# Performance work log

Hardware: AMD Instinct MI355X
Metric: run time of the kernel (lower is better)

The kernel has to match this reference:

```python
import jax, jax.numpy as jnp
import numpy as np
import math

B, S, T = 32, 128, 64
FEAT = 16
H = 1024
V = 32000


def _gru_step(x, h, wih, whh, bih, bhh):
    # torch nn.GRU cell: gates ordered (r, z, n)
    gi = x @ wih.T + bih
    gh = h @ whh.T + bhh
    ir, iz, in_ = jnp.split(gi, 3, axis=-1)
    hr, hz, hn = jnp.split(gh, 3, axis=-1)
    r = jax.nn.sigmoid(ir + hr)
    z = jax.nn.sigmoid(iz + hz)
    n = jnp.tanh(in_ + r * hn)
    return (1.0 - z) * n + z * h


def _forward(features, target_tokens, temp_W, temp_b, hum_W, hum_b, cloud_W, cloud_b,
             time_W, time_b, other_W, other_b, fi_W, fi_b,
             enc_wih, enc_whh, enc_bih, enc_bhh, emb, attn_W, attn_b,
             dec_wih, dec_whh, dec_bih, dec_bhh, out_W, out_b):
    b = features.shape[0]
    # per-feature projections (dropout = identity in eval mode)
    temp = features[:, :, 0:1] @ temp_W.T + temp_b
    hum = features[:, :, 1:2] @ hum_W.T + hum_b
    cloud = features[:, :, 2:3] @ cloud_W.T + cloud_b
    time = features[:, :, -5:-3] @ time_W.T + time_b
    other_in = jnp.concatenate([features[:, :, 3:-5], features[:, :, -3:]], axis=2)
    other = other_in @ other_W.T + other_b
    concat = jnp.concatenate([temp, hum, cloud, time, other], axis=2)  # [B,S,2H]
    proj = jnp.tanh(concat @ fi_W.T + fi_b)  # [B,S,H]

    # encoder GRU over time
    def enc_step(h, x):
        h2 = _gru_step(x, h, enc_wih, enc_whh, enc_bih, enc_bhh)
        return h2, h2
    h0 = jnp.zeros((b, H), proj.dtype)
    h_last, enc_outs = jax.lax.scan(enc_step, h0, proj.transpose(1, 0, 2))
    enc_out = enc_outs.transpose(1, 0, 2)  # [B,S,H]

    # attention keys computed once (loop-invariant in the original)
    keys = enc_out @ attn_W.T + attn_b  # [B,S,H]
    scale = 1.0 / math.sqrt(H)

    # decoder: teacher_forcing_ratio = 1.0 -> input at step t is target_tokens[:, t-1]
    def dec_step(h, tok):
        e = emb[tok]  # [B,H]
        scores = jnp.einsum('bh,bsh->bs', h, keys) * scale
        w = jax.nn.softmax(scores, axis=-1)
        ctx = jnp.einsum('bs,bsh->bh', w, enc_out)
        x = jnp.concatenate([e, ctx], axis=-1)  # [B,2H]
        h2 = _gru_step(x, h, dec_wih, dec_whh, dec_bih, dec_bhh)
        pred = jnp.concatenate([h2, ctx], axis=-1) @ out_W.T + out_b  # [B,V]
        return h2, pred

    _, preds = jax.lax.scan(dec_step, h_last, target_tokens[:, :-1].T)  # [T-1,B,V]
    outputs = jnp.zeros((b, target_tokens.shape[1], V), preds.dtype)
    outputs = outputs.at[:, 0, target_tokens[0, 0]].set(1.0)
    outputs = outputs.at[:, 1:, :].set(preds.transpose(1, 0, 2))
    return outputs


def setup_inputs() -> dict:
    key = jax.random.key(0)
    ks = jax.random.split(key, 32)
    nrm = lambda k, sh: jax.random.normal(k, sh, jnp.float32) * 0.05
    Hq = H // 4
    d = {}
    d['features'] = jax.random.normal(ks[0], (B, S, FEAT), jnp.float32)
    d['target_tokens'] = jax.random.randint(ks[1], (B, T), 0, V, dtype=jnp.int32)
    d['temp_W'] = nrm(ks[2], (Hq, 1)); d['temp_b'] = nrm(ks[3], (Hq,))
    d['hum_W'] = nrm(ks[4], (Hq, 1)); d['hum_b'] = nrm(ks[5], (Hq,))
    d['cloud_W'] = nrm(ks[6], (Hq, 1)); d['cloud_b'] = nrm(ks[7], (Hq,))
    d['time_W'] = nrm(ks[8], (Hq, 2)); d['time_b'] = nrm(ks[9], (Hq,))
    d['other_W'] = nrm(ks[10], (H, FEAT - 5)); d['other_b'] = nrm(ks[11], (H,))
    d['fi_W'] = nrm(ks[12], (H, 2 * H)); d['fi_b'] = nrm(ks[13], (H,))
    d['enc_wih'] = nrm(ks[14], (3 * H, H)); d['enc_whh'] = nrm(ks[15], (3 * H, H))
    d['enc_bih'] = nrm(ks[16], (3 * H,)); d['enc_bhh'] = nrm(ks[17], (3 * H,))
    d['emb'] = nrm(ks[18], (V, H))
    d['attn_W'] = nrm(ks[19], (H, H)); d['attn_b'] = nrm(ks[20], (H,))
    d['dec_wih'] = nrm(ks[21], (3 * H, 2 * H)); d['dec_whh'] = nrm(ks[22], (3 * H, H))
    d['dec_bih'] = nrm(ks[23], (3 * H,)); d['dec_bhh'] = nrm(ks[24], (3 * H,))
    d['out_W'] = nrm(ks[25], (V, 2 * H)); d['out_b'] = nrm(ks[26], (V,))
    return d


def reference(features, target_tokens, temp_W, temp_b, hum_W, hum_b, cloud_W, cloud_b,
              time_W, time_b, other_W, other_b, fi_W, fi_b,
              enc_wih, enc_whh, enc_bih, enc_bhh, emb, attn_W, attn_b,
              dec_wih, dec_whh, dec_bih, dec_bhh, out_W, out_b):
    return _forward(features, target_tokens, temp_W, temp_b, hum_W, hum_b, cloud_W, cloud_b,
                    time_W, time_b, other_W, other_b, fi_W, fi_b,
                    enc_wih, enc_whh, enc_bih, enc_bhh, emb, attn_W, attn_b,
                    dec_wih, dec_whh, dec_bih, dec_bhh, out_W, out_b)
```

## Files before the change

### kernel.cpp

```cpp
#include <hip/hip_runtime.h>

typedef float f32x4 __attribute__((ext_vector_type(4)));
typedef __bf16 bf16x8 __attribute__((ext_vector_type(8)));

#define DI static __device__ __forceinline__

DI unsigned short f2bf(float f) {
  unsigned u = __float_as_uint(f);
  u = (u + 0x7fffu + ((u >> 16) & 1u)) >> 16;
  return (unsigned short)u;
}
DI unsigned pk2(float lo, float hi) {
  return (unsigned)f2bf(lo) | ((unsigned)f2bf(hi) << 16);
}
DI float bflo(unsigned u) { return __uint_as_float(u << 16); }
DI float bfhi(unsigned u) { return __uint_as_float(u & 0xffff0000u); }
DI float sigm(float x) { return 1.0f / (1.0f + expf(-x)); }

DI void gl_lds16(const unsigned short* g, unsigned short* l) {
  __builtin_amdgcn_global_load_lds(
      (const __attribute__((address_space(1))) unsigned int*)g,
      (__attribute__((address_space(3))) unsigned int*)l, 16, 0, 0);
}

DI void st32_sc1(unsigned* p, unsigned v) {
  __hip_atomic_store(p, v, __ATOMIC_RELAXED, __HIP_MEMORY_SCOPE_AGENT);
}
DI void st64_sc1(unsigned long long* p, unsigned long long v) {
  __hip_atomic_store(p, v, __ATOMIC_RELAXED, __HIP_MEMORY_SCOPE_AGENT);
}
DI int ldw(const int* p) {
  return __hip_atomic_load(p, __ATOMIC_RELAXED, __HIP_MEMORY_SCOPE_AGENT);
}
DI void stw(int* p, int v) {
  __hip_atomic_store(p, v, __ATOMIC_RELAXED, __HIP_MEMORY_SCOPE_AGENT);
}

DI void burn(int n) {
  float x = (float)(int)threadIdx.x;
#pragma unroll 1
  for (int i = 0; i < n; ++i) x = __builtin_fmaf(x, 1.0000001f, 1e-9f);
  asm volatile("" :: "v"(x));
}

DI void waitrel(const int* relbase, int repl, int target) {
  const int* w = relbase + repl * 32;
  for (;;) {
    int v = 0;
    if ((threadIdx.x & 63) == 0) v = ldw(w);
    v = __shfl(v, 0);
    if (v >= target) break;
    burn(60);
  }
  asm volatile("" ::: "memory");
}
DI void strel(int* relbase, int v) {
  int l = threadIdx.x & 63;
  if (l < 8) stw(relbase + l * 32, v);
}
DI void wait_arr32(const int* arr, int target) {
  const int l = (int)(threadIdx.x & 63);
  const int* p = arr + (l << 3);
  for (;;) {
    int v = (l < 32) ? ldw(p) : target;
    if (__all(v >= target)) break;
    burn(60);
  }
  asm volatile("" ::: "memory");
}

__global__ void k_fold(const float* __restrict__ tW, const float* __restrict__ tb,
                       const float* __restrict__ hW, const float* __restrict__ hb,
                       const float* __restrict__ cW, const float* __restrict__ cb,
                       const float* __restrict__ tiW, const float* __restrict__ tib,
                       const float* __restrict__ oW, const float* __restrict__ ob,
                       const float* __restrict__ fiW, const float* __restrict__ fib,
                       float* __restrict__ M, float* __restrict__ b0v)
{
  int g = blockIdx.x * 256 + threadIdx.x;
  if (g >= 1024 * 17) return;
  int h = g / 17, f = g - h * 17;
  const float* fw = fiW + (size_t)h * 2048;
  float s = 0.f;
  if (f == 16) {
    for (int k = 0; k < 256; ++k) s += fw[k] * tb[k];
    for (int k = 0; k < 256; ++k) s += fw[256 + k] * hb[k];
    for (int k = 0; k < 256; ++k) s += fw[512 + k] * cb[k];
    for (int k = 0; k < 256; ++k) s += fw[768 + k] * tib[k];
    for (int r = 0; r < 1024; ++r) s += fw[1024 + r] * ob[r];
    b0v[h] = s + fib[h];
  } else if (f == 0) {
    for (int k = 0; k < 256; ++k) s += fw[k] * tW[k];
    M[h * 16 + 0] = s;
  } else if (f == 1) {
    for (int k = 0; k < 256; ++k) s += fw[256 + k] * hW[k];
    M[h * 16 + 1] = s;
  } else if (f == 2) {
    for (int k = 0; k < 256; ++k) s += fw[512 + k] * cW[k];
    M[h * 16 + 2] = s;
  } else if (f == 11) {
    for (int k = 0; k < 256; ++k) s += fw[768 + k] * tiW[2 * k];
    M[h * 16 + 11] = s;
  } else if (f == 12) {
    for (int k = 0; k < 256; ++k) s += fw[768 + k] * tiW[2 * k + 1];
    M[h * 16 + 12] = s;
  } else {
    int col = (f <= 10) ? (f - 3) : (f - 5);
    for (int r = 0; r < 1024; ++r) s += fw[1024 + r] * oW[r * 11 + col];
    M[h * 16 + f] = s;
  }
}

__global__ __launch_bounds__(256)
void k_proj(const float* __restrict__ feat, const float* __restrict__ M,
            const float* __restrict__ b0v, unsigned short* __restrict__ proj)
{
  __shared__ float ft[16];
  int bs = blockIdx.x;
  int h = blockIdx.y * 256 + threadIdx.x;
  if (threadIdx.x < 16) ft[threadIdx.x] = feat[bs * 16 + threadIdx.x];
  __syncthreads();
  float sum = b0v[h];
  const float* mr = M + h * 16;
#pragma unroll
  for (int f = 0; f < 16; ++f) sum += mr[f] * ft[f];
  proj[(size_t)bs * 1024 + h] = f2bf(tanhf(sum));
}

__global__ void k_conv(const float* __restrict__ s, unsigned short* __restrict__ d, int n8)
{
  for (long i = (long)blockIdx.x * 256 + threadIdx.x; i < n8; i += (long)gridDim.x * 256) {
    const float* p = s + i * 8;
    f32x4 a = *(const f32x4*)p, b = *(const f32x4*)(p + 4);
    uint4 o;
    o.x = pk2(a[0], a[1]); o.y = pk2(a[2], a[3]);
    o.z = pk2(b[0], b[1]); o.w = pk2(b[2], b[3]);
    *(uint4*)(d + i * 8) = o;
  }
}

__global__ void k_conv_str(const float* __restrict__ s, unsigned short* __restrict__ d, int coff)
{
  int r = blockIdx.x;
  int c = threadIdx.x * 4;
  f32x4 a = *(const f32x4*)(s + (size_t)r * 2048 + coff + c);
  uint2 o; o.x = pk2(a[0], a[1]); o.y = pk2(a[2], a[3]);
  *(uint2*)(d + (size_t)r * 1024 + c) = o;
}

__global__ void k_gather_e(const int* __restrict__ toks, const float* __restrict__ emb,
                           unsigned short* __restrict__ e_bf)
{
  int row = blockIdx.x;
  int t = row >> 5, b = row & 31;
  unsigned short* dst = e_bf + (size_t)row * 1024 + threadIdx.x * 4;
  if (t < 63) {
    int tok = toks[b * 64 + t];
    f32x4 a = *(const f32x4*)(emb + (size_t)tok * 1024 + threadIdx.x * 4);
    uint2 o; o.x = pk2(a[0], a[1]); o.y = pk2(a[2], a[3]);
    *(uint2*)dst = o;
  } else {
    uint2 o; o.x = 0u; o.y = 0u;
    *(uint2*)dst = o;
  }
}

__global__ void k_onehot(const int* __restrict__ toks, float* __restrict__ out)
{
  int i = blockIdx.x * 256 + threadIdx.x;
  if (i >= 32 * 32000) return;
  int b = i / 32000, v = i - b * 32000;
  out[(size_t)b * 64 * 32000 + v] = (v == toks[0]) ? 1.0f : 0.0f;
}

template<int MODE>
__global__ __launch_bounds__(256)
void gemm_bf(const unsigned short* __restrict__ A, const unsigned short* __restrict__ B,
             const float* __restrict__ bias, float* __restrict__ Cf,
             unsigned short* __restrict__ Cb,
             int tiles_m, int K, int lda, int ldb, int ldc, int coloff)
{
  __shared__ unsigned short As[4096];
  __shared__ unsigned short Bs[4096];
  const int nblk = gridDim.x;
  const int cpx = nblk >> 3;
  const int bid = blockIdx.x;
  const int id = (bid & 7) * cpx + (bid >> 3);
  const int tm = id % tiles_m, tn = id / tiles_m;
  const int tid = threadIdx.x;
  const int lane = tid & 63, wave = tid >> 6;
  const int wm = (wave & 1) << 6, wn = (wave >> 1) << 6;
  const int r0 = tid >> 2, kc0 = (tid & 3) << 3;
  const unsigned short* ga0 = A + (size_t)(tm * 128 + r0) * lda + kc0;
  const unsigned short* ga1 = A + (size_t)(tm * 128 + 64 + r0) * lda + kc0;
  const unsigned short* gb0 = B + (size_t)(tn * 128 + r0) * ldb + kc0;
  const unsigned short* gb1 = B + (size_t)(tn * 128 + 64 + r0) * ldb + kc0;
  const int lr = lane & 15, lkb = (lane >> 4) << 3;

  f32x4 acc[4][4];
#pragma unroll
  for (int m = 0; m < 4; ++m)
#pragma unroll
    for (int n = 0; n < 4; ++n) { acc[m][n][0]=0.f; acc[m][n][1]=0.f; acc[m][n][2]=0.f; acc[m][n][3]=0.f; }

  for (int kt = 0; kt < K; kt += 32) {
    __syncthreads();
    gl_lds16(ga0 + kt, &As[tid * 8]);
    gl_lds16(ga1 + kt, &As[(tid + 256) * 8]);
    gl_lds16(gb0 + kt, &Bs[tid * 8]);
    gl_lds16(gb1 + kt, &Bs[(tid + 256) * 8]);
    __syncthreads();
    bf16x8 af[4], bfv[4];
#pragma unroll
    for (int m = 0; m < 4; ++m) af[m] = *(const bf16x8*)&As[(wm + m * 16 + lr) * 32 + lkb];
#pragma unroll
    for (int n = 0; n < 4; ++n) bfv[n] = *(const bf16x8*)&Bs[(wn + n * 16 + lr) * 32 + lkb];
#pragma unroll
    for (int m = 0; m < 4; ++m)
#pragma unroll
      for (int n = 0; n < 4; ++n)
        acc[m][n] = __builtin_amdgcn_mfma_f32_16x16x32_bf16(af[m], bfv[n], acc[m][n], 0, 0, 0);
  }

#pragma unroll
  for (int m = 0; m < 4; ++m) {
    int rb = tm * 128 + wm + m * 16 + ((lane >> 4) << 2);
#pragma unroll
    for (int n = 0; n < 4; ++n) {
      int c = tn * 128 + wn + n * 16 + lr;
      float bb = bias[c];
#pragma unroll
      for (int i = 0; i < 4; ++i) {
        float v = acc[m][n][i] + bb;
        int r = rb + i;
        if (MODE == 0) {
          Cf[(size_t)r * ldc + c] = v;
        } else if (MODE == 1) {
          Cb[(size_t)r * ldc + c] = f2bf(v);
        } else if (MODE == 3) {
          Cb[(size_t)c * 4096 + r] = f2bf(v);
        } else {
          if (r < 2016) {
            int t = r >> 5, b2 = r & 31;
            Cf[((size_t)b2 * 64 + t + 1) * 32000 + coloff + c] = v;
          }
        }
      }
    }
  }
}

__global__ __launch_bounds__(256, 1)
void k_enc_scan(const float* __restrict__ gi_all, const float* __restrict__ whh,
                const float* __restrict__ bhh, float* __restrict__ hfp,
                unsigned short* __restrict__ enc_bf,
                int* __restrict__ arrE, int* __restrict__ relE)
{
  const int tid = threadIdx.x;
  const int blk = blockIdx.x;
  if (blk == 64) {
    if (tid < 64) {
      for (int g = 1; g <= 127; ++g) {
        for (;;) {
          int v = ldw(&arrE[tid << 3]);
          if (__all(v >= g)) break;
          burn(60);
        }
        asm volatile("" ::: "memory");
        strel(relE, g);
      }
    }
    return;
  }

  __shared__ unsigned short W[48 * 1024];
  __shared__ float Cred[4 * 2 * 3 * 64 * 4];
  const int lane = tid & 63, wave = tid >> 6;
  const int j0 = blk * 16;
  const int repl = blk & 7;

  for (int i = tid; i < 48 * 128; i += 256) {
    int r = i >> 7, c = i & 127;
    int gr = ((r >> 4) << 10) + j0 + (r & 15);
    const float* src = whh + ((size_t)gr << 10) + (c << 3);
    f32x4 a = *(const f32x4*)src, b = *(const f32x4*)(src + 4);
    uint4 o;
    o.x = pk2(a[0], a[1]); o.y = pk2(a[2], a[3]);
    o.z = pk2(b[0], b[1]); o.w = pk2(b[2], b[3]);
    *(uint4*)&W[(r << 10) + ((c ^ (r & 7)) << 3)] = o;
  }
  __syncthreads();

  int cb[2], cj[2], clb[2], creg[2], cm[2];
  float bh0[2], bh1[2], bh2[2];
  float hp[2] = {0.f, 0.f};
#pragma unroll
  for (int cc = 0; cc < 2; ++cc) {
    int cell = tid + (cc << 8);
    cb[cc] = cell >> 4; cj[cc] = cell & 15;
    clb[cc] = ((cb[cc] & 15) >> 2) * 16;
    creg[cc] = cb[cc] & 3; cm[cc] = cb[cc] >> 4;
    bh0[cc] = bhh[j0 + cj[cc]];
    bh1[cc] = bhh[1024 + j0 + cj[cc]];
    bh2[cc] = bhh[2048 + j0 + cj[cc]];
  }

#pragma unroll 1
  for (int s = 0; s < 128; ++s) {
    float gp[2][3];
#pragma unroll
    for (int cc = 0; cc < 2; ++cc) {
      const float* gi = gi_all + ((size_t)cb[cc] * 128 + s) * 3072 + j0 + cj[cc];
      gp[cc][0] = gi[0]; gp[cc][1] = gi[1024]; gp[cc][2] = gi[2048];
    }

    f32x4 acc[2][3];
#pragma unroll
    for (int m = 0; m < 2; ++m)
#pragma unroll
      for (int n = 0; n < 3; ++n) { acc[m][n][0]=0.f; acc[m][n][1]=0.f; acc[m][n][2]=0.f; acc[m][n][3]=0.f; }

    if (s > 0) {
      waitrel(relE, repl, s);
      const unsigned short* hr = enc_bf + (size_t)(s - 1) * 1024;
      const int k0 = wave << 8;
      bf16x8 af[2][8];
#pragma unroll
      for (int kk = 0; kk < 8; ++kk) {
        int k = k0 + kk * 32 + ((lane >> 4) << 3);
        af[0][kk] = *(const bf16x8*)(hr + (size_t)(lane & 15) * 131072 + k);
        af[1][kk] = *(const bf16x8*)(hr + (size_t)(16 + (lane & 15)) * 131072 + k);
      }
#pragma unroll
      for (int kk = 0; kk < 8; ++kk) {
        int c = ((k0 + kk * 32) >> 3) + (lane >> 4);
#pragma unroll
        for (int n = 0; n < 3; ++n) {
          int wr = n * 16 + (lane & 15);
          bf16x8 bfr = *(const bf16x8*)&W[(wr << 10) + ((c ^ (wr & 7)) << 3)];
          acc[0][n] = __builtin_amdgcn_mfma_f32_16x16x32_bf16(af[0][kk], bfr, acc[0][n], 0, 0, 0);
          acc[1][n] = __builtin_amdgcn_mfma_f32_16x16x32_bf16(af[1][kk], bfr, acc[1][n], 0, 0, 0);
        }
      }
    }
#pragma unroll
    for (int m = 0; m < 2; ++m)
#pragma unroll
      for (int n = 0; n < 3; ++n)
        *(f32x4*)&Cred[((((wave * 2 + m) * 3 + n) * 64) + lane) << 2] = acc[m][n];
    __syncthreads();

    float h2v[2];
#pragma unroll
    for (int cc = 0; cc < 2; ++cc) {
      int lj = clb[cc] + cj[cc], reg = creg[cc], m = cm[cc];
      float Cr = 0.f, Cz = 0.f, Cn = 0.f;
#pragma unroll
      for (int w = 0; w < 4; ++w) {
        Cr += Cred[((((w * 2 + m) * 3 + 0) * 64 + lj) << 2) + reg];
        Cz += Cred[((((w * 2 + m) * 3 + 1) * 64 + lj) << 2) + reg];
        Cn += Cred[((((w * 2 + m) * 3 + 2) * 64 + lj) << 2) + reg];
      }
      float r = sigm(gp[cc][0] + Cr + bh0[cc]);
      float z = sigm(gp[cc][1] + Cz + bh1[cc]);
      float n = tanhf(gp[cc][2] + r * (Cn + bh2[cc]));
      float h2 = (1.f - z) * n + z * hp[cc];
      h2v[cc] = h2; hp[cc] = h2;
    }
    if (s == 127) {
      hfp[cb[0] * 1024 + j0 + cj[0]] = h2v[0];
      hfp[cb[1] * 1024 + j0 + cj[1]] = h2v[1];
    }
#pragma unroll
    for (int cc = 0; cc < 2; ++cc) {
      unsigned short sv = f2bf(h2v[cc]);
      unsigned p = (unsigned)sv | (((unsigned)__shfl_xor((int)(unsigned)sv, 1)) << 16);
      unsigned q = (unsigned)__shfl_xor((int)p, 2);
      if ((tid & 3) == 0) {
        unsigned long long dv = (unsigned long long)p | ((unsigned long long)q << 32);
        st64_sc1((unsigned long long*)&enc_bf[((size_t)cb[cc] * 128 + s) * 1024 + j0 + cj[cc]], dv);
      }
    }
    __syncthreads();
    if (tid == 0) stw(&arrE[blk << 3], s + 1);
  }
}

__global__ __launch_bounds__(256, 1)
void k_dec_scan(const float* __restrict__ gi_e, const float* __restrict__ whh,
                const float* __restrict__ bhh,
                const unsigned short* __restrict__ keys,
                const unsigned short* __restrict__ enc_bf,
                unsigned short* __restrict__ hcat, const float* __restrict__ hfp0,
                const unsigned short* __restrict__ xeT, float* __restrict__ w_all,
                int* __restrict__ arrW, int* __restrict__ arrH,
                int* __restrict__ relH)
{
  const int tid = threadIdx.x;
  const int blk = blockIdx.x;
  const int repl = blk & 7;

  if (blk == 160) {
    if (tid < 64) {
      for (int g = 1; g <= 62; ++g) {
        for (;;) {
          int v0 = ldw(&arrH[(tid * 2) << 4]);
          int v1 = ldw(&arrH[(tid * 2 + 1) << 4]);
          if (__all(v0 >= g && v1 >= g)) break;
          burn(60);
        }
        asm volatile("" ::: "memory");
        strel(relH, g);
      }
    }
    return;
  }

  if (blk < 32) {
    __shared__ unsigned short hsh[1024];
    __shared__ float sarr[128];
    __shared__ float earr[128];
    const int b = blk;
#pragma unroll 1
    for (int t = 0; t < 63; ++t) {
      if (t) waitrel(relH, repl, t);
      const unsigned short* hsrc = (t == 0)
          ? (enc_bf + (size_t)b * 131072 + (size_t)127 * 1024)
          : (hcat + ((size_t)(t - 1) * 32 + b) * 2048);
      *(uint2*)&hsh[tid * 4] = *(const uint2*)(hsrc + tid * 4);
      __syncthreads();
      {
        int sp = tid >> 1, kh = (tid & 1) << 9;
        const unsigned short* kr = keys + ((size_t)b * 128 + sp) * 1024 + kh;
        float a0 = 0.f, a1 = 0.f, a2 = 0.f, a3 = 0.f;
#pragma unroll 8
        for (int c = 0; c < 512; c += 8) {
          uint4 kv = *(const uint4*)(kr + c);
          uint4 hv = *(const uint4*)&hsh[kh + c];
          a0 += bflo(kv.x) * bflo(hv.x) + bfhi(kv.x) * bfhi(hv.x);
          a1 += bflo(kv.y) * bflo(hv.y) + bfhi(kv.y) * bfhi(hv.y);
          a2 += bflo(kv.z) * bflo(hv.z) + bfhi(kv.z) * bfhi(hv.z);
          a3 += bflo(kv.w) * bflo(hv.w) + bfhi(kv.w) * bfhi(hv.w);
        }
        float a = (a0 + a1) + (a2 + a3);
        a += __shfl_xor(a, 1);
        if ((tid & 1) == 0) sarr[sp] = a * 0.03125f;
      }
      __syncthreads();
      float m0 = -1e30f, m1 = -1e30f, m2 = -1e30f, m3 = -1e30f;
#pragma unroll 8
      for (int i2 = 0; i2 < 128; i2 += 4) {
        m0 = fmaxf(m0, sarr[i2]); m1 = fmaxf(m1, sarr[i2 + 1]);
        m2 = fmaxf(m2, sarr[i2 + 2]); m3 = fmaxf(m3, sarr[i2 + 3]);
      }
      float mx = fmaxf(fmaxf(m0, m1), fmaxf(m2, m3));
      if (tid < 128) earr[tid] = expf(sarr[tid] - mx);
      __syncthreads();
      float s0 = 0.f, s1 = 0.f, s2 = 0.f, s3 = 0.f;
#pragma unroll 8
      for (int i2 = 0; i2 < 128; i2 += 4) {
        s0 += earr[i2]; s1 += earr[i2 + 1]; s2 += earr[i2 + 2]; s3 += earr[i2 + 3];
      }
      float winv = 1.f / ((s0 + s1) + (s2 + s3));
      if (tid < 64) {
        unsigned lo = __float_as_uint(earr[tid * 2] * winv);
        unsigned hi = __float_as_uint(earr[tid * 2 + 1] * winv);
        st64_sc1((unsigned long long*)(w_all + ((size_t)t * 32 + b) * 128 + tid * 2),
                 (unsigned long long)lo | ((unsigned long long)hi << 32));
      }
      __syncthreads();
      if (tid == 0) stw(&arrW[b << 3], t + 1);
      f32x4 cacc; cacc[0]=0.f; cacc[1]=0.f; cacc[2]=0.f; cacc[3]=0.f;
      const unsigned short* eb = enc_bf + ((size_t)b << 17) + tid * 4;
#pragma unroll 4
      for (int s2i = 0; s2i < 128; ++s2i) {
        float w = earr[s2i] * winv;
        uint2 ev = *(const uint2*)(eb + ((size_t)s2i << 10));
        cacc[0] += w * bflo(ev.x); cacc[1] += w * bfhi(ev.x);
        cacc[2] += w * bflo(ev.y); cacc[3] += w * bfhi(ev.y);
      }
      uint2 co; co.x = pk2(cacc[0], cacc[1]); co.y = pk2(cacc[2], cacc[3]);
      *(uint2*)(hcat + ((size_t)t * 32 + b) * 2048 + 1024 + tid * 4) = co;
    }
    return;
  }

  __shared__ unsigned short Wh[32 * 1024];
  __shared__ float Cred[4 * 2 * 2 * 64 * 4];
  const int lane = tid & 63, wave = tid >> 6;
  const int gblk = blk - 32;
  const int j0 = gblk * 8;

  for (int i = tid; i < 32 * 128; i += 256) {
    int r = i >> 7, c = i & 127;
    int off = (r << 10) + ((c ^ (r & 7)) << 3);
    uint4 oh;
    oh.x = oh.y = oh.z = oh.w = 0u;
    if (r < 24) {
      int gr = ((r >> 3) << 10) + j0 + (r & 7);
      const float* sh = whh + ((size_t)gr << 10) + (c << 3);
      f32x4 a = *(const f32x4*)sh, b = *(const f32x4*)(sh + 4);
      oh.x = pk2(a[0], a[1]); oh.y = pk2(a[2], a[3]);
      oh.z = pk2(b[0], b[1]); oh.w = pk2(b[2], b[3]);
    }
    *(uint4*)&Wh[off] = oh;
  }
  __syncthreads();

  const int gb = tid >> 3, gj = tid & 7;
  const int glb = ((gb & 15) >> 2) * 16;
  const int greg = gb & 3, gm = gb >> 4;
  const float bh0 = bhh[j0 + gj];
  const float bh1 = bhh[1024 + j0 + gj];
  const float bh2 = bhh[2048 + j0 + gj];
  float hpv = hfp0[gb * 1024 + j0 + gj];
  const unsigned short* x0 = xeT + ((size_t)(j0 + gj) << 12) + gb * 128;
  const unsigned short* x1 = xeT + ((size_t)(1024 + j0 + gj) << 12) + gb * 128;
  const unsigned short* x2 = xeT + ((size_t)(2048 + j0 + gj) << 12) + gb * 128;

#pragma unroll 1
  for (int t = 0; t < 63; ++t) {
    const float* gie = gi_e + ((size_t)t * 32 + gb) * 3072 + j0 + gj;
    float g0 = gie[0], g1 = gie[1024], g2 = gie[2048];

    if (t) waitrel(relH, repl, t);
    const unsigned short* abase;
    size_t astr;
    if (t == 0) { abase = enc_bf + (size_t)127 * 1024; astr = 131072; }
    else { abase = hcat + (size_t)(t - 1) * 32 * 2048; astr = 2048; }
    const int k0 = wave << 8;
    f32x4 acc[2][2];
#pragma unroll
    for (int m = 0; m < 2; ++m)
#pragma unroll
      for (int n = 0; n < 2; ++n) { acc[m][n][0]=0.f; acc[m][n][1]=0.f; acc[m][n][2]=0.f; acc[m][n][3]=0.f; }
    {
      bf16x8 af[2][8];
#pragma unroll
      for (int kk = 0; kk < 8; ++kk) {
        int k = k0 + kk * 32 + ((lane >> 4) << 3);
        af[0][kk] = *(const bf16x8*)(abase + (size_t)(lane & 15) * astr + k);
        af[1][kk] = *(const bf16x8*)(abase + (size_t)(16 + (lane & 15)) * astr + k);
      }
#pragma unroll
      for (int kk = 0; kk < 8; ++kk) {
        int c = ((k0 + kk * 32) >> 3) + (lane >> 4);
#pragma unroll
        for (int n = 0; n < 2; ++n) {
          int wr = n * 16 + (lane & 15);
          bf16x8 bfr = *(const bf16x8*)&Wh[(wr << 10) + ((c ^ (wr & 7)) << 3)];
          acc[0][n] = __builtin_amdgcn_mfma_f32_16x16x32_bf16(af[0][kk], bfr, acc[0][n], 0, 0, 0);
          acc[1][n] = __builtin_amdgcn_mfma_f32_16x16x32_bf16(af[1][kk], bfr, acc[1][n], 0, 0, 0);
        }
      }
    }
#pragma unroll
    for (int m = 0; m < 2; ++m)
#pragma unroll
      for (int n = 0; n < 2; ++n)
        *(f32x4*)&Cred[((((wave * 2 + m) * 2 + n) * 64) + lane) << 2] = acc[m][n];
    __syncthreads();

    wait_arr32(arrW, t + 1);
    float cx0 = 0.f, cx1 = 0.f, cx2 = 0.f;
    const float* wrow = w_all + ((size_t)t * 32 + gb) * 128;
#pragma unroll 4
    for (int s = 0; s < 128; s += 8) {
      f32x4 wa = *(const f32x4*)(wrow + s);
      f32x4 wb2 = *(const f32x4*)(wrow + s + 4);
      uint4 a0 = *(const uint4*)(x0 + s);
      uint4 a1 = *(const uint4*)(x1 + s);
      uint4 a2 = *(const uint4*)(x2 + s);
      cx0 += wa[0]*bflo(a0.x) + wa[1]*bfhi(a0.x) + wa[2]*bflo(a0.y) + wa[3]*bfhi(a0.y)
           + wb2[0]*bflo(a0.z) + wb2[1]*bfhi(a0.z) + wb2[2]*bflo(a0.w) + wb2[3]*bfhi(a0.w);
      cx1 += wa[0]*bflo(a1.x) + wa[1]*bfhi(a1.x) + wa[2]*bflo(a1.y) + wa[3]*bfhi(a1.y)
           + wb2[0]*bflo(a1.z) + wb2[1]*bfhi(a1.z) + wb2[2]*bflo(a1.w) + wb2[3]*bfhi(a1.w);
      cx2 += wa[0]*bflo(a2.x) + wa[1]*bfhi(a2.x) + wa[2]*bflo(a2.y) + wa[3]*bfhi(a2.y)
           + wb2[0]*bflo(a2.z) + wb2[1]*bfhi(a2.z) + wb2[2]*bflo(a2.w) + wb2[3]*bfhi(a2.w);
    }

    {
      float Chr = 0.f, Chz = 0.f, Chn = 0.f;
#pragma unroll
      for (int w = 0; w < 4; ++w) {
        Chr += Cred[((((w * 2 + gm) * 2 + 0) * 64 + glb + gj) << 2) + greg];
        Chz += Cred[((((w * 2 + gm) * 2 + 0) * 64 + glb + gj + 8) << 2) + greg];
        Chn += Cred[((((w * 2 + gm) * 2 + 1) * 64 + glb + gj) << 2) + greg];
      }
      float r = sigm(g0 + cx0 + Chr + bh0);
      float z = sigm(g1 + cx1 + Chz + bh1);
      float n2 = tanhf(g2 + cx2 + r * (Chn + bh2));
      float h2 = (1.f - z) * n2 + z * hpv;
      hpv = h2;
      unsigned short sv = f2bf(h2);
      unsigned p = (unsigned)sv | (((unsigned)__shfl_xor((int)(unsigned)sv, 1)) << 16);
      unsigned q = (unsigned)__shfl_xor((int)p, 2);
      if ((tid & 3) == 0) {
        unsigned long long dv = (unsigned long long)p | ((unsigned long long)q << 32);
        st64_sc1((unsigned long long*)&hcat[((size_t)t * 32 + gb) * 2048 + j0 + gj], dv);
      }
    }
    __syncthreads();
    if (tid == 0) stw(&arrH[gblk << 4], t + 1);
  }
}

extern "C" void kernel_launch(void* const* d_in, const int* in_sizes, int n_in,
                              void* d_out, int out_size, void* d_ws, size_t ws_size,
                              hipStream_t stream)
{
  const float* features = (const float*)d_in[0];
  const int*   toks     = (const int*)d_in[1];
  const float* temp_W = (const float*)d_in[2];  const float* temp_b = (const float*)d_in[3];
  const float* hum_W  = (const float*)d_in[4];  const float* hum_b  = (const float*)d_in[5];
  const float* cloud_W= (const float*)d_in[6];  const float* cloud_b= (const float*)d_in[7];
  const float* time_W = (const float*)d_in[8];  const float* time_b = (const float*)d_in[9];
  const float* other_W= (const float*)d_in[10]; const float* other_b= (const float*)d_in[11];
  const float* fi_W   = (const float*)d_in[12]; const float* fi_b   = (const float*)d_in[13];
  const float* enc_wih= (const float*)d_in[14]; const float* enc_whh= (const float*)d_in[15];
  const float* enc_bih= (const float*)d_in[16]; const float* enc_bhh= (const float*)d_in[17];
  const float* emb    = (const float*)d_in[18];
  const float* attn_W = (const float*)d_in[19]; const float* attn_b = (const float*)d_in[20];
  const float* dec_wih= (const float*)d_in[21]; const float* dec_whh= (const float*)d_in[22];
  const float* dec_bih= (const float*)d_in[23]; const float* dec_bhh= (const float*)d_in[24];
  const float* out_W  = (const float*)d_in[25]; const float* out_b  = (const float*)d_in[26];
  float* out = (float*)d_out;
  char* ws = (char*)d_ws;

  int*            arrE    = (int*)(ws + 0);
  int*            arrH    = (int*)(ws + 4096);
  int*            arrW    = (int*)(ws + 12288);
  int*            relE    = (int*)(ws + 14336);
  int*            relH    = (int*)(ws + 15360);
  float*          zbias   = (float*)(ws + 16384);
  float*          Mf      = (float*)(ws + 32768);
  float*          b0v     = (float*)(ws + 98304);
  float*          hfp     = (float*)(ws + 102400);
  unsigned short* hcat    = (unsigned short*)(ws + 233472);
  unsigned short* keys_bf = (unsigned short*)(ws + 8622080);
  unsigned short* enc_bf  = (unsigned short*)(ws + 17010688);
  float*          w_all   = (float*)(ws + 25399296);
  float*          gi_e    = (float*)(ws + 26447872);
  unsigned short* xeT     = (unsigned short*)(ws + 51613696);
  float*          gi_all  = (float*)(ws + 76779520);
  unsigned short* proj_bf = (unsigned short*)(ws + 127111168);
  unsigned short* e_bf    = (unsigned short*)(ws + 135499776);
  unsigned short* wihE_bf = (unsigned short*)(ws + 139694080);
  unsigned short* attnW_bf= (unsigned short*)(ws + 145985536);
  unsigned short* wihD_bf = (unsigned short*)(ws + 148082688);
  unsigned short* wihDc_bf= (unsigned short*)(ws + 154374144);
  unsigned short* outW_bf = (unsigned short*)(ws + 26447872);

  hipMemsetAsync(ws, 0, 32768, stream);
  hipMemsetAsync(ws + 233472 + (size_t)2016 * 2048 * 2, 0, 32 * 2048 * 2, stream);

  k_conv<<<1536, 256, 0, stream>>>(enc_wih, wihE_bf, 393216);
  k_conv<<<512, 256, 0, stream>>>(attn_W, attnW_bf, 131072);
  k_conv_str<<<3072, 256, 0, stream>>>(dec_wih, wihD_bf, 0);
  k_conv_str<<<3072, 256, 0, stream>>>(dec_wih, wihDc_bf, 1024);

  k_fold<<<68, 256, 0, stream>>>(temp_W, temp_b, hum_W, hum_b, cloud_W, cloud_b,
                                 time_W, time_b, other_W, other_b, fi_W, fi_b, Mf, b0v);
  k_proj<<<dim3(4096, 4), 256, 0, stream>>>(features, Mf, b0v, proj_bf);

  gemm_bf<0><<<768, 256, 0, stream>>>(proj_bf, wihE_bf, enc_bih, gi_all, nullptr,
                                      32, 1024, 1024, 1024, 3072, 0);
  k_enc_scan<<<65, 256, 0, stream>>>(gi_all, enc_whh, enc_bhh, hfp, enc_bf, arrE, relE);

  gemm_bf<1><<<256, 256, 0, stream>>>(enc_bf, attnW_bf, attn_b, nullptr, keys_bf,
                                      32, 1024, 1024, 1024, 1024, 0);
  k_gather_e<<<2048, 256, 0, stream>>>(toks, emb, e_bf);
  gemm_bf<0><<<384, 256, 0, stream>>>(e_bf, wihD_bf, dec_bih, gi_e, nullptr,
                                      16, 1024, 1024, 1024, 3072, 0);
  gemm_bf<3><<<768, 256, 0, stream>>>(enc_bf, wihDc_bf, zbias, nullptr, xeT,
                                      32, 1024, 1024, 1024, 0, 0);
  k_dec_scan<<<161, 256, 0, stream>>>(gi_e, dec_whh, dec_bhh, keys_bf, enc_bf,
                                      hcat, hfp, xeT, w_all, arrW, arrH, relH);

  k_conv<<<2048, 256, 0, stream>>>(out_W, outW_bf, 4096000);
  gemm_bf<2><<<2000, 256, 0, stream>>>(hcat, outW_bf, out_b, out, nullptr,
                                       16, 2048, 2048, 2048, 0, 0);
  k_conv<<<2048, 256, 0, stream>>>(out_W + (size_t)16000 * 2048, outW_bf, 4096000);
  gemm_bf<2><<<2000, 256, 0, stream>>>(hcat, outW_bf, out_b + 16000, out, nullptr,
                                       16, 2048, 2048, 2048, 0, 16000);
  k_onehot<<<4000, 256, 0, stream>>>(toks, out);
}
```

Baseline: 2.910 ms.

## Split attention across blocks, cache keys in LDS, defer context to separate kernel

The decoder scan now uses two attention blocks per batch row, each holding 64 key rows in swizzled LDS, and writes unnormalized exp scores without a max subtraction. The per-step context computation over enc_out is moved out of the serial loop into a new batched k_ctx kernel. The GRU blocks keep xeT rows in registers and normalize by the score sum themselves. A relay block now publishes two-phase release counters for the attention and hidden-state stages. The aim is to shorten the serial critical path per step, at the cost of softmax overflow risk without the max subtraction and higher register pressure.

```diff
diff --git a/kernel.cpp b/kernel.cpp
--- a/kernel.cpp
+++ b/kernel.cpp
@@ -57,16 +57,6 @@
 DI void strel(int* relbase, int v) {
   int l = threadIdx.x & 63;
   if (l < 8) stw(relbase + l * 32, v);
-}
-DI void wait_arr32(const int* arr, int target) {
-  const int l = (int)(threadIdx.x & 63);
-  const int* p = arr + (l << 3);
-  for (;;) {
-    int v = (l < 32) ? ldw(p) : target;
-    if (__all(v >= target)) break;
-    burn(60);
-  }
-  asm volatile("" ::: "memory");
 }
 
 __global__ void k_fold(const float* __restrict__ tW, const float* __restrict__ tb,
@@ -394,101 +384,97 @@
                 unsigned short* __restrict__ hcat, const float* __restrict__ hfp0,
                 const unsigned short* __restrict__ xeT, float* __restrict__ w_all,
                 int* __restrict__ arrW, int* __restrict__ arrH,
-                int* __restrict__ relH)
-{
+                int* __restrict__ relD)
+{
+  static __shared__ __attribute__((aligned(16))) char smem[135168];
   const int tid = threadIdx.x;
   const int blk = blockIdx.x;
   const int repl = blk & 7;
 
-  if (blk == 160) {
+  if (blk == 192) {
     if (tid < 64) {
-      for (int g = 1; g <= 62; ++g) {
+      for (int t = 0; t < 63; ++t) {
+        for (;;) {
+          int v = ldw(&arrW[tid << 3]);
+          if (__all(v >= t + 1)) break;
+          burn(60);
+        }
+        asm volatile("" ::: "memory");
+        strel(relD, 2 * t + 1);
         for (;;) {
           int v0 = ldw(&arrH[(tid * 2) << 4]);
           int v1 = ldw(&arrH[(tid * 2 + 1) << 4]);
-          if (__all(v0 >= g && v1 >= g)) break;
+          if (__all(v0 >= t + 1 && v1 >= t + 1)) break;
           burn(60);
         }
         asm volatile("" ::: "memory");
-        strel(relH, g);
+        strel(relD, 2 * t + 2);
       }
     }
     return;
   }
 
-  if (blk < 32) {
-    __shared__ unsigned short hsh[1024];
-    __shared__ float sarr[128];
-    __shared__ float earr[128];
-    const int b = blk;
+  if (blk < 64) {
+    unsigned short* Ks = (unsigned short*)smem;
+    unsigned short* hsh = (unsigned short*)(smem + 131072);
+    float* parr = (float*)(smem + 133120);
+    const int b = blk >> 1, half = blk & 1;
+    const int lane = tid & 63, wave = tid >> 6;
+
+    for (int i = tid; i < 64 * 128; i += 256) {
+      int s = i >> 7, c = i & 127;
+      uint4 kv = *(const uint4*)(keys + ((size_t)(b * 128 + half * 64 + s) << 10) + (c << 3));
+      *(uint4*)&Ks[(s << 10) + ((c ^ (s & 7)) << 3)] = kv;
+    }
+    __syncthreads();
+
 #pragma unroll 1
     for (int t = 0; t < 63; ++t) {
-      if (t) waitrel(relH, repl, t);
+      if (t) waitrel(relD, repl, 2 * t);
       const unsigned short* hsrc = (t == 0)
           ? (enc_bf + (size_t)b * 131072 + (size_t)127 * 1024)
           : (hcat + ((size_t)(t - 1) * 32 + b) * 2048);
       *(uint2*)&hsh[tid * 4] = *(const uint2*)(hsrc + tid * 4);
       __syncthreads();
-      {
-        int sp = tid >> 1, kh = (tid & 1) << 9;
-        const unsigned short* kr = keys + ((size_t)b * 128 + sp) * 1024 + kh;
-        float a0 = 0.f, a1 = 0.f, a2 = 0.f, a3 = 0.f;
+      float a0 = 0.f, a1 = 0.f;
 #pragma unroll 8
-        for (int c = 0; c < 512; c += 8) {
-          uint4 kv = *(const uint4*)(kr + c);
-          uint4 hv = *(const uint4*)&hsh[kh + c];
-          a0 += bflo(kv.x) * bflo(hv.x) + bfhi(kv.x) * bfhi(hv.x);
-          a1 += bflo(kv.y) * bflo(hv.y) + bfhi(kv.y) * bfhi(hv.y);
-          a2 += bflo(kv.z) * bflo(hv.z) + bfhi(kv.z) * bfhi(hv.z);
-          a3 += bflo(kv.w) * bflo(hv.w) + bfhi(kv.w) * bfhi(hv.w);
+      for (int i = 0; i < 32; i += 2) {
+        int c0 = wave * 32 + i, c1 = c0 + 1;
+        uint4 kv0 = *(const uint4*)&Ks[(lane << 10) + ((c0 ^ (lane & 7)) << 3)];
+        uint4 kv1 = *(const uint4*)&Ks[(lane << 10) + ((c1 ^ (lane & 7)) << 3)];
+        uint4 hv0 = *(const uint4*)&hsh[c0 << 3];
+        uint4 hv1 = *(const uint4*)&hsh[c1 << 3];
+        a0 += bflo(kv0.x) * bflo(hv0.x) + bfhi(kv0.x) * bfhi(hv0.x)
+            + bflo(kv0.y) * bflo(hv0.y) + bfhi(kv0.y) * bfhi(hv0.y)
+            + bflo(kv0.z) * bflo(hv0.z) + bfhi(kv0.z) * bfhi(hv0.z)
+            + bflo(kv0.w) * bflo(hv0.w) + bfhi(kv0.w) * bfhi(hv0.w);
+        a1 += bflo(kv1.x) * bflo(hv1.x) + bfhi(kv1.x) * bfhi(hv1.x)
+            + bflo(kv1.y) * bflo(hv1.y) + bfhi(kv1.y) * bfhi(hv1.y)
+            + bflo(kv1.z) * bflo(hv1.z) + bfhi(kv1.z) * bfhi(hv1.z)
+            + bflo(kv1.w) * bflo(hv1.w) + bfhi(kv1.w) * bfhi(hv1.w);
+      }
+      parr[wave * 64 + lane] = a0 + a1;
+      __syncthreads();
+      if (tid < 64) {
+        float sc = (parr[tid] + parr[64 + tid] + parr[128 + tid] + parr[192 + tid]) * 0.03125f;
+        float e = expf(sc);
+        float eo = __shfl_xor(e, 1);
+        if ((tid & 1) == 0) {
+          unsigned long long dv = (unsigned long long)__float_as_uint(e)
+                                | ((unsigned long long)__float_as_uint(eo) << 32);
+          st64_sc1((unsigned long long*)(w_all + ((size_t)t * 32 + b) * 128 + half * 64 + tid), dv);
         }
-        float a = (a0 + a1) + (a2 + a3);
-        a += __shfl_xor(a, 1);
-        if ((tid & 1) == 0) sarr[sp] = a * 0.03125f;
       }
       __syncthreads();
-      float m0 = -1e30f, m1 = -1e30f, m2 = -1e30f, m3 = -1e30f;
-#pragma unroll 8
-      for (int i2 = 0; i2 < 128; i2 += 4) {
-        m0 = fmaxf(m0, sarr[i2]); m1 = fmaxf(m1, sarr[i2 + 1]);
-        m2 = fmaxf(m2, sarr[i2 + 2]); m3 = fmaxf(m3, sarr[i2 + 3]);
-      }
-      float mx = fmaxf(fmaxf(m0, m1), fmaxf(m2, m3));
-      if (tid < 128) earr[tid] = expf(sarr[tid] - mx);
-      __syncthreads();
-      float s0 = 0.f, s1 = 0.f, s2 = 0.f, s3 = 0.f;
-#pragma unroll 8
-      for (int i2 = 0; i2 < 128; i2 += 4) {
-        s0 += earr[i2]; s1 += earr[i2 + 1]; s2 += earr[i2 + 2]; s3 += earr[i2 + 3];
-      }
-      float winv = 1.f / ((s0 + s1) + (s2 + s3));
-      if (tid < 64) {
-        unsigned lo = __float_as_uint(earr[tid * 2] * winv);
-        unsigned hi = __float_as_uint(earr[tid * 2 + 1] * winv);
-        st64_sc1((unsigned long long*)(w_all + ((size_t)t * 32 + b) * 128 + tid * 2),
-                 (unsigned long long)lo | ((unsigned long long)hi << 32));
-      }
-      __syncthreads();
-      if (tid == 0) stw(&arrW[b << 3], t + 1);
-      f32x4 cacc; cacc[0]=0.f; cacc[1]=0.f; cacc[2]=0.f; cacc[3]=0.f;
-      const unsigned short* eb = enc_bf + ((size_t)b << 17) + tid * 4;
-#pragma unroll 4
-      for (int s2i = 0; s2i < 128; ++s2i) {
-        float w = earr[s2i] * winv;
-        uint2 ev = *(const uint2*)(eb + ((size_t)s2i << 10));
-        cacc[0] += w * bflo(ev.x); cacc[1] += w * bfhi(ev.x);
-        cacc[2] += w * bflo(ev.y); cacc[3] += w * bfhi(ev.y);
-      }
-      uint2 co; co.x = pk2(cacc[0], cacc[1]); co.y = pk2(cacc[2], cacc[3]);
-      *(uint2*)(hcat + ((size_t)t * 32 + b) * 2048 + 1024 + tid * 4) = co;
+      if (tid == 0) stw(&arrW[blk << 3], t + 1);
     }
     return;
   }
 
-  __shared__ unsigned short Wh[32 * 1024];
-  __shared__ float Cred[4 * 2 * 2 * 64 * 4];
+  unsigned short* Wh = (unsigned short*)smem;
+  float* Cred = (float*)(smem + 65536);
   const int lane = tid & 63, wave = tid >> 6;
-  const int gblk = blk - 32;
+  const int gblk = blk - 64;
   const int j0 = gblk * 8;
 
   for (int i = tid; i < 32 * 128; i += 256) {
@@ -514,16 +500,26 @@
   const float bh1 = bhh[1024 + j0 + gj];
   const float bh2 = bhh[2048 + j0 + gj];
   float hpv = hfp0[gb * 1024 + j0 + gj];
-  const unsigned short* x0 = xeT + ((size_t)(j0 + gj) << 12) + gb * 128;
-  const unsigned short* x1 = xeT + ((size_t)(1024 + j0 + gj) << 12) + gb * 128;
-  const unsigned short* x2 = xeT + ((size_t)(2048 + j0 + gj) << 12) + gb * 128;
+
+  uint4 x0v[16], x1v[16], x2v[16];
+  {
+    const unsigned short* x0 = xeT + ((size_t)(j0 + gj) << 12) + gb * 128;
+    const unsigned short* x1 = xeT + ((size_t)(1024 + j0 + gj) << 12) + gb * 128;
+    const unsigned short* x2 = xeT + ((size_t)(2048 + j0 + gj) << 12) + gb * 128;
+#pragma unroll
+    for (int i = 0; i < 16; ++i) {
+      x0v[i] = *(const uint4*)(x0 + i * 8);
+      x1v[i] = *(const uint4*)(x1 + i * 8);
+      x2v[i] = *(const uint4*)(x2 + i * 8);
+    }
+  }
 
 #pragma unroll 1
   for (int t = 0; t < 63; ++t) {
     const float* gie = gi_e + ((size_t)t * 32 + gb) * 3072 + j0 + gj;
     float g0 = gie[0], g1 = gie[1024], g2 = gie[2048];
 
-    if (t) waitrel(relH, repl, t);
+    if (t) waitrel(relD, repl, 2 * t);
     const unsigned short* abase;
     size_t astr;
     if (t == 0) { abase = enc_bf + (size_t)127 * 1024; astr = 131072; }
@@ -561,16 +557,15 @@
         *(f32x4*)&Cred[((((wave * 2 + m) * 2 + n) * 64) + lane) << 2] = acc[m][n];
     __syncthreads();
 
-    wait_arr32(arrW, t + 1);
-    float cx0 = 0.f, cx1 = 0.f, cx2 = 0.f;
+    waitrel(relD, repl, 2 * t + 1);
     const float* wrow = w_all + ((size_t)t * 32 + gb) * 128;
-#pragma unroll 4
-    for (int s = 0; s < 128; s += 8) {
-      f32x4 wa = *(const f32x4*)(wrow + s);
-      f32x4 wb2 = *(const f32x4*)(wrow + s + 4);
-      uint4 a0 = *(const uint4*)(x0 + s);
-      uint4 a1 = *(const uint4*)(x1 + s);
-      uint4 a2 = *(const uint4*)(x2 + s);
+    float se = 0.f, cx0 = 0.f, cx1 = 0.f, cx2 = 0.f;
+#pragma unroll
+    for (int i = 0; i < 16; ++i) {
+      f32x4 wa = *(const f32x4*)(wrow + i * 8);
+      f32x4 wb2 = *(const f32x4*)(wrow + i * 8 + 4);
+      se += (wa[0] + wa[1]) + (wa[2] + wa[3]) + (wb2[0] + wb2[1]) + (wb2[2] + wb2[3]);
+      uint4 a0 = x0v[i], a1 = x1v[i], a2 = x2v[i];
       cx0 += wa[0]*bflo(a0.x) + wa[1]*bfhi(a0.x) + wa[2]*bflo(a0.y) + wa[3]*bfhi(a0.y)
            + wb2[0]*bflo(a0.z) + wb2[1]*bfhi(a0.z) + wb2[2]*bflo(a0.w) + wb2[3]*bfhi(a0.w);
       cx1 += wa[0]*bflo(a1.x) + wa[1]*bfhi(a1.x) + wa[2]*bflo(a1.y) + wa[3]*bfhi(a1.y)
@@ -578,6 +573,8 @@
       cx2 += wa[0]*bflo(a2.x) + wa[1]*bfhi(a2.x) + wa[2]*bflo(a2.y) + wa[3]*bfhi(a2.y)
            + wb2[0]*bflo(a2.z) + wb2[1]*bfhi(a2.z) + wb2[2]*bflo(a2.w) + wb2[3]*bfhi(a2.w);
     }
+    float inv = 1.f / se;
+    cx0 *= inv; cx1 *= inv; cx2 *= inv;
 
     {
       float Chr = 0.f, Chz = 0.f, Chn = 0.f;
@@ -602,6 +599,54 @@
     }
     __syncthreads();
     if (tid == 0) stw(&arrH[gblk << 4], t + 1);
+  }
+}
+
+__global__ __launch_bounds__(256)
+void k_ctx(const float* __restrict__ w_all, const unsigned short* __restrict__ enc_bf,
+           unsigned short* __restrict__ hcat)
+{
+  __shared__ float wsh[8][128];
+  __shared__ float inv[8];
+  const int b = blockIdx.x, tg = blockIdx.y;
+  const int t0 = tg * 8;
+  const int nt = (t0 + 8 <= 63) ? 8 : (63 - t0);
+  const int tid = threadIdx.x;
+  for (int idx = tid; idx < 8 * 128; idx += 256) {
+    int tt = idx >> 7, s = idx & 127;
+    wsh[tt][s] = (tt < nt) ? w_all[((size_t)(t0 + tt) * 32 + b) * 128 + s] : 0.f;
+  }
+  __syncthreads();
+  if (tid < 8) {
+    float s = 0.f;
+    for (int i = 0; i < 128; ++i) s += wsh[tid][i];
+    inv[tid] = (tid < nt) ? 1.f / s : 0.f;
+  }
+  __syncthreads();
+  const int j0 = tid * 4;
+  f32x4 cacc[8];
+#pragma unroll
+  for (int tt = 0; tt < 8; ++tt) { cacc[tt][0]=0.f; cacc[tt][1]=0.f; cacc[tt][2]=0.f; cacc[tt][3]=0.f; }
+  const unsigned short* eb = enc_bf + ((size_t)b << 17) + j0;
+  for (int s = 0; s < 128; ++s) {
+    uint2 ev = *(const uint2*)(eb + ((size_t)s << 10));
+    float v0 = bflo(ev.x), v1 = bfhi(ev.x), v2 = bflo(ev.y), v3 = bfhi(ev.y);
+#pragma unroll
+    for (int tt = 0; tt < 8; ++tt) {
+      float w = wsh[tt][s];
+      cacc[tt][0] += w * v0; cacc[tt][1] += w * v1;
+      cacc[tt][2] += w * v2; cacc[tt][3] += w * v3;
+    }
+  }
+#pragma unroll
+  for (int tt = 0; tt < 8; ++tt) {
+    if (tt < nt) {
+      float iv = inv[tt];
+      uint2 co;
+      co.x = pk2(cacc[tt][0] * iv, cacc[tt][1] * iv);
+      co.y = pk2(cacc[tt][2] * iv, cacc[tt][3] * iv);
+      *(uint2*)(hcat + ((size_t)(t0 + tt) * 32 + b) * 2048 + 1024 + j0) = co;
+    }
   }
 }
 
@@ -631,7 +676,7 @@
   int*            arrH    = (int*)(ws + 4096);
   int*            arrW    = (int*)(ws + 12288);
   int*            relE    = (int*)(ws + 14336);
-  int*            relH    = (int*)(ws + 15360);
+  int*            relD    = (int*)(ws + 15360);
   float*          zbias   = (float*)(ws + 16384);
   float*          Mf      = (float*)(ws + 32768);
   float*          b0v     = (float*)(ws + 98304);
@@ -674,8 +719,9 @@
                                       16, 1024, 1024, 1024, 3072, 0);
   gemm_bf<3><<<768, 256, 0, stream>>>(enc_bf, wihDc_bf, zbias, nullptr, xeT,
                                       32, 1024, 1024, 1024, 0, 0);
-  k_dec_scan<<<161, 256, 0, stream>>>(gi_e, dec_whh, dec_bhh, keys_bf, enc_bf,
-                                      hcat, hfp, xeT, w_all, arrW, arrH, relH);
+  k_dec_scan<<<193, 256, 0, stream>>>(gi_e, dec_whh, dec_bhh, keys_bf, enc_bf,
+                                      hcat, hfp, xeT, w_all, arrW, arrH, relD);
+  k_ctx<<<dim3(32, 8), 256, 0, stream>>>(w_all, enc_bf, hcat);
 
   k_conv<<<2048, 256, 0, stream>>>(out_W, outW_bf, 4096000);
   gemm_bf<2><<<2000, 256, 0, stream>>>(hcat, outW_bf, out_b, out, nullptr,
```

Result: faster. 2.617 ms (median of 2 runs) (-10.1%).
